# Kernel tuning notes

Measured on AMD Instinct MI355X. Metric: run time of the kernel, lower is better.

The kernel has to match this reference:

```python
import jax, jax.numpy as jnp
import numpy as np

FEAT = 1024
B = 1024
S = 64


def setup_inputs() -> dict:
    key = jax.random.key(0)
    ks = jax.random.split(key, 6)
    scale_ih = 1.0 / np.sqrt(2 * FEAT)
    scale_hh = 1.0 / np.sqrt(FEAT)
    return {
        "query": jax.random.normal(ks[0], (B, FEAT), jnp.float32) * 0.1,
        "support_context": jax.random.normal(ks[1], (S, FEAT), jnp.float32) * 0.1,
        "W_ih": jax.random.normal(ks[2], (4 * FEAT, 2 * FEAT), jnp.float32) * scale_ih,
        "W_hh": jax.random.normal(ks[3], (4 * FEAT, FEAT), jnp.float32) * scale_hh,
        "b_ih": jax.random.normal(ks[4], (4 * FEAT,), jnp.float32) * scale_hh,
        "b_hh": jax.random.normal(ks[5], (4 * FEAT,), jnp.float32) * scale_hh,
    }


def reference(query, support_context, W_ih, W_hh, b_ih, b_hh):
    # query: [B, F]; support_context: [S, F]; steps == S
    hidden = query
    cell = jnp.zeros_like(query)
    support_t = support_context.T  # [F, S]

    def step(carry, _):
        h, c = carry
        attn = jax.nn.softmax(h @ support_t, axis=1)          # [B, S]
        readout = attn @ support_context                      # [B, F]
        x = jnp.concatenate([query, readout], axis=1)         # [B, 2F]
        gates = x @ W_ih.T + b_ih + h @ W_hh.T + b_hh          # [B, 4F]
        i, f, g, o = jnp.split(gates, 4, axis=1)               # torch LSTMCell gate order
        c_new = jax.nn.sigmoid(f) * c + jax.nn.sigmoid(i) * jnp.tanh(g)
        h_new = jax.nn.sigmoid(o) * jnp.tanh(c_new) + query   # skip connection per original
        return (h_new, c_new), None

    (hidden, cell), _ = jax.lax.scan(step, (hidden, cell), None,
                                     length=support_context.shape[0])
    return hidden
```

## Files before the change

### kernel.cpp

```cpp
#include <hip/hip_runtime.h>
#include <hip/hip_bf16.h>


typedef __attribute__((ext_vector_type(8))) __bf16 bf16x8;
typedef __attribute__((ext_vector_type(4))) float f32x4;
typedef __attribute__((ext_vector_type(8))) unsigned short ushort8;

__device__ __forceinline__ ushort f2bf(float f) {
  union { float f; unsigned int u; } v; v.f = f;
  unsigned int u = v.u;
  u += 0x7FFFu + ((u >> 16) & 1u);
  return (ushort)(u >> 16);
}
__device__ __forceinline__ float bf2f(ushort u) {
  union { float f; unsigned int u; } v; v.u = ((unsigned int)u) << 16; return v.f;
}
__device__ __forceinline__ float sigm_(float x) { return 1.f / (1.f + __expf(-x)); }
__device__ __forceinline__ float tanh_(float x) {
  x = fminf(15.f, fmaxf(-15.f, x));
  float e = __expf(2.f * x);
  return (e - 1.f) / (e + 1.f);
}
__device__ __forceinline__ void async16(ushort* lds, const ushort* g) {
  __builtin_amdgcn_global_load_lds(
      (const __attribute__((address_space(1))) void*)g,
      (__attribute__((address_space(3))) void*)lds, 16, 0, 0);
}
__device__ __forceinline__ int permrow(int n) {
  int g = n >> 10, j = n & 1023;
  return ((j >> 4) << 6) | (g << 4) | (j & 15);
}

__global__ __launch_bounds__(256) void prep_kernel(
    const float* __restrict__ query, const float* __restrict__ support,
    const float* __restrict__ W_ih, const float* __restrict__ W_hh,
    const float* __restrict__ b_ih, const float* __restrict__ b_hh,
    ushort* __restrict__ Wq_bf, ushort* __restrict__ Wcomb,
    float* __restrict__ bias_p, ushort* __restrict__ X0,
    float* __restrict__ c, float* __restrict__ sT)
{
  int g = blockIdx.x * 256 + threadIdx.x;
  int n = g >> 10, k = g & 1023;
  int np = permrow(n);
  Wq_bf[(size_t)np * 1024 + k] = f2bf(W_ih[(size_t)n * 2048 + k]);
  Wcomb[(size_t)np * 1088 + k] = f2bf(W_hh[(size_t)n * 1024 + k]);
  if (g < 1024 * 1024) {
    X0[(size_t)(g >> 10) * 1088 + (g & 1023)] = f2bf(query[g]);
    c[g] = 0.f;
  }
  if (g < 4096) bias_p[permrow(g)] = b_ih[g] + b_hh[g];
  if (g < 65536) { int kk = g >> 6, s = g & 63; sT[g] = support[(size_t)s * 1024 + kk]; }
}

__global__ __launch_bounds__(256) void sw_kernel(
    const float* __restrict__ sT, const float* __restrict__ W_ih,
    ushort* __restrict__ Wcomb)
{
  int g = blockIdx.x * 256 + threadIdx.x;
  int n = g >> 6, s = g & 63;
  const float* wp = W_ih + (size_t)n * 2048 + 1024;
  const float* sp = sT + s;
  float a0 = 0.f, a1 = 0.f, a2 = 0.f, a3 = 0.f;
#pragma unroll 4
  for (int k = 0; k < 1024; k += 4) {
    a0 += wp[k]     * sp[(size_t)(k)     * 64];
    a1 += wp[k + 1] * sp[(size_t)(k + 1) * 64];
    a2 += wp[k + 2] * sp[(size_t)(k + 2) * 64];
    a3 += wp[k + 3] * sp[(size_t)(k + 3) * 64];
  }
  Wcomb[(size_t)permrow(n) * 1088 + 1024 + s] = f2bf((a0 + a1) + (a2 + a3));
}

__global__ __launch_bounds__(256) void attn_kernel(
    const ushort* __restrict__ Xh, const float* __restrict__ sT,
    ushort* __restrict__ Xa)
{
  __shared__ float hs[2][1024];
  __shared__ float part[4][2][64];
  int t = threadIdx.x;
  int b0 = blockIdx.x * 2;
  {
    int r = t >> 7, c8 = (t & 127) << 3;
    ushort8 v = *(const ushort8*)&Xh[(size_t)(b0 + r) * 1088 + c8];
#pragma unroll
    for (int i = 0; i < 8; i++) hs[r][c8 + i] = bf2f(v[i]);
  }
  __syncthreads();
  int s = t & 63, q = t >> 6;
  const float* st = sT + (size_t)q * 256 * 64 + s;
  const float* h0 = &hs[0][q * 256];
  const float* h1 = &hs[1][q * 256];
  float a0 = 0.f, a1 = 0.f;
#pragma unroll 8
  for (int k = 0; k < 256; k++) {
    float sv = st[(size_t)k * 64];
    a0 += h0[k] * sv; a1 += h1[k] * sv;
  }
  part[q][0][s] = a0; part[q][1][s] = a1;
  __syncthreads();
  if (t < 64) {
#pragma unroll
    for (int r = 0; r < 2; r++) {
      float v = part[0][r][t] + part[1][r][t] + part[2][r][t] + part[3][r][t];
      float m = v;
      for (int off = 32; off; off >>= 1) m = fmaxf(m, __shfl_xor(m, off));
      float e = __expf(v - m);
      float sm = e;
      for (int off = 32; off; off >>= 1) sm += __shfl_xor(sm, off);
      Xa[(size_t)(b0 + r) * 1088 + 1024 + t] = f2bf(e / sm);
    }
  }
}

__global__ __launch_bounds__(256) void gemm_step(
    const ushort* __restrict__ A, const ushort* __restrict__ Bw,
    int lda, int ldb, int K,
    const float* __restrict__ base, const float* __restrict__ bias,
    float* __restrict__ Cout,
    float* __restrict__ cbuf, const float* __restrict__ query,
    ushort* __restrict__ Xout, float* __restrict__ outp)
{
  __shared__ ushort As[3][64 * 32];
  __shared__ ushort Bs[3][128 * 32];
  const int t = threadIdx.x;
  const int bid = blockIdx.x;
  const int xcd = bid & 7, idx = bid >> 3;
  const int bx = idx & 15, byy = idx >> 4;
  const int by = xcd * 4 + byy;
  const int m0 = bx * 64, n0 = by * 128;
  const int w = t >> 6, l = t & 63;
  const int wm = (w >> 1) * 32, wn = (w & 1) * 64;
  const int srow = t >> 2, scol = (t & 3) * 8;
  const ushort* ga  = A  + (size_t)(m0 + srow) * lda + scol;
  const ushort* gb0 = Bw + (size_t)(n0 + srow) * ldb + scol;
  const ushort* gb1 = Bw + (size_t)(n0 + 64 + srow) * ldb + scol;
  const int fr = l & 15, fk = (l >> 4) * 8, fq = l >> 4;
  f32x4 acc[2][4] = {};
  const int nt = K >> 5;
  {
    async16(&As[0][t * 8], ga);
    async16(&Bs[0][t * 8], gb0);
    async16(&Bs[0][2048 + t * 8], gb1);
    async16(&As[1][t * 8], ga + 32);
    async16(&Bs[1][t * 8], gb0 + 32);
    async16(&Bs[1][2048 + t * 8], gb1 + 32);
  }
  for (int it = 0; it < nt; it++) {
    if (it + 1 < nt) { asm volatile("s_waitcnt vmcnt(3)" ::: "memory"); }
    else             { asm volatile("s_waitcnt vmcnt(0)" ::: "memory"); }
    __builtin_amdgcn_s_barrier();
    __builtin_amdgcn_sched_barrier(0);
    const int b = it % 3;
    const ushort* pa = &As[b][(wm + fr) * 32 + fk];
    const ushort* pb = &Bs[b][(wn + fr) * 32 + fk];
    bf16x8 af[2], bfv[4];
#pragma unroll
    for (int mi = 0; mi < 2; mi++) af[mi] = *(const bf16x8*)(pa + mi * 512);
#pragma unroll
    for (int ni = 0; ni < 4; ni++) bfv[ni] = *(const bf16x8*)(pb + ni * 512);
    if (it + 2 < nt) {
      const int pbuf = (it + 2) % 3;
      const int k0 = (it + 2) << 5;
      async16(&As[pbuf][t * 8], ga + k0);
      async16(&Bs[pbuf][t * 8], gb0 + k0);
      async16(&Bs[pbuf][2048 + t * 8], gb1 + k0);
    }
#pragma unroll
    for (int mi = 0; mi < 2; mi++)
#pragma unroll
      for (int ni = 0; ni < 4; ni++)
        acc[mi][ni] = __builtin_amdgcn_mfma_f32_16x16x32_bf16(af[mi], bfv[ni], acc[mi][ni], 0, 0, 0);
  }
  if (!base) {
#pragma unroll
    for (int mi = 0; mi < 2; mi++)
#pragma unroll
      for (int ni = 0; ni < 4; ni++) {
        int col = n0 + wn + ni * 16 + fr;
        int row0 = m0 + wm + mi * 16 + fq * 4;
        float bv = bias[col];
#pragma unroll
        for (int jj = 0; jj < 4; jj++)
          Cout[(size_t)(row0 + jj) * 4096 + col] = acc[mi][ni][jj] + bv;
      }
    return;
  }
  const int jbase = (((n0 + wn) >> 6) << 4);
  const int jcol = jbase + fr;
#pragma unroll
  for (int mi = 0; mi < 2; mi++) {
#pragma unroll
    for (int jj = 0; jj < 4; jj++) {
      int row = m0 + wm + mi * 16 + fq * 4 + jj;
      const float* bp = base + (size_t)row * 4096 + (n0 + wn);
      float gi = acc[mi][0][jj] + bp[fr];
      float gf = acc[mi][1][jj] + bp[16 + fr];
      float gg = acc[mi][2][jj] + bp[32 + fr];
      float go = acc[mi][3][jj] + bp[48 + fr];
      size_t cidx = (size_t)row * 1024 + jcol;
      float cv = cbuf[cidx];
      float cn = sigm_(gf) * cv + sigm_(gi) * tanh_(gg);
      float hn = sigm_(go) * tanh_(cn) + query[cidx];
      cbuf[cidx] = cn;
      Xout[(size_t)row * 1088 + jcol] = f2bf(hn);
      if (outp) outp[cidx] = hn;
    }
  }
}

extern "C" void kernel_launch(void* const* d_in, const int* in_sizes, int n_in,
                              void* d_out, int out_size, void* d_ws, size_t ws_size,
                              hipStream_t stream) {
  const float* query   = (const float*)d_in[0];
  const float* support = (const float*)d_in[1];
  const float* W_ih    = (const float*)d_in[2];
  const float* W_hh    = (const float*)d_in[3];
  const float* b_ih    = (const float*)d_in[4];
  const float* b_hh    = (const float*)d_in[5];
  float* out = (float*)d_out;

  char* ws = (char*)d_ws;
  size_t off = 0;
  auto alloc = [&](size_t bytes) {
    void* p = ws + off;
    off += (bytes + 255) & ~(size_t)255;
    return p;
  };
  ushort* Wq_bf  = (ushort*)alloc((size_t)4096 * 1024 * 2);
  ushort* Wcomb  = (ushort*)alloc((size_t)4096 * 1088 * 2);
  float*  bias_p = (float*) alloc((size_t)4096 * 4);
  float*  base   = (float*) alloc((size_t)1024 * 4096 * 4);
  ushort* X0     = (ushort*)alloc((size_t)1024 * 1088 * 2);
  ushort* X1     = (ushort*)alloc((size_t)1024 * 1088 * 2);
  float*  c      = (float*) alloc((size_t)1024 * 1024 * 4);
  float*  sT     = (float*) alloc((size_t)1024 * 64 * 4);

  prep_kernel<<<16384, 256, 0, stream>>>(query, support, W_ih, W_hh, b_ih, b_hh,
                                         Wq_bf, Wcomb, bias_p, X0, c, sT);
  sw_kernel<<<1024, 256, 0, stream>>>(sT, W_ih, Wcomb);
  gemm_step<<<512, 256, 0, stream>>>(X0, Wq_bf, 1088, 1024, 1024,
                                     nullptr, bias_p, base,
                                     nullptr, nullptr, nullptr, nullptr);
  for (int step = 0; step < 64; step++) {
    ushort* Xc = (step & 1) ? X1 : X0;
    ushort* Xn = (step & 1) ? X0 : X1;
    attn_kernel<<<512, 256, 0, stream>>>(Xc, sT, Xc);
    gemm_step<<<512, 256, 0, stream>>>(Xc, Wcomb, 1088, 1088, 1088,
                                       base, nullptr, nullptr,
                                       c, query, Xn,
                                       (step == 63) ? out : nullptr);
  }
}
```

Before: 2.176 ms.

## Enlarge GEMM tiles, use MFMA for support-weight fold, batch four rows per attention block

The per-step gemm_step tile grows from 64x128 to 128x128 with four MFMA row fragments per wave, halving the grid to 256 blocks and raising operand reuse per LDS load. The scalar sw_kernel that folds W_ih's readout half with the support matrix is replaced by a bf16 MFMA kernel, which needs extra bf16 copies of that weight and the support. attn_kernel now handles four batch rows per block with float4 LDS reads and all four waves doing softmax. The larger tiles cut parallelism to 256 blocks, about one per CU, which may leave latency less hidden.

```diff
diff --git a/kernel.cpp b/kernel.cpp
--- a/kernel.cpp
+++ b/kernel.cpp
@@ -37,78 +37,133 @@
     const float* __restrict__ b_ih, const float* __restrict__ b_hh,
     ushort* __restrict__ Wq_bf, ushort* __restrict__ Wcomb,
     float* __restrict__ bias_p, ushort* __restrict__ X0,
-    float* __restrict__ c, float* __restrict__ sT)
+    float* __restrict__ c, float* __restrict__ sT,
+    ushort* __restrict__ Wr_bf, ushort* __restrict__ Sb)
 {
   int g = blockIdx.x * 256 + threadIdx.x;
   int n = g >> 10, k = g & 1023;
   int np = permrow(n);
   Wq_bf[(size_t)np * 1024 + k] = f2bf(W_ih[(size_t)n * 2048 + k]);
+  Wr_bf[(size_t)n * 1024 + k]  = f2bf(W_ih[(size_t)n * 2048 + 1024 + k]);
   Wcomb[(size_t)np * 1088 + k] = f2bf(W_hh[(size_t)n * 1024 + k]);
   if (g < 1024 * 1024) {
     X0[(size_t)(g >> 10) * 1088 + (g & 1023)] = f2bf(query[g]);
     c[g] = 0.f;
   }
   if (g < 4096) bias_p[permrow(g)] = b_ih[g] + b_hh[g];
-  if (g < 65536) { int kk = g >> 6, s = g & 63; sT[g] = support[(size_t)s * 1024 + kk]; }
-}
-
-__global__ __launch_bounds__(256) void sw_kernel(
-    const float* __restrict__ sT, const float* __restrict__ W_ih,
+  if (g < 65536) {
+    int kk = g >> 6, s = g & 63;
+    float v = support[(size_t)s * 1024 + kk];
+    sT[g] = v;
+    Sb[(size_t)s * 1024 + kk] = f2bf(v);
+  }
+}
+
+__global__ __launch_bounds__(256) void sw_mfma(
+    const ushort* __restrict__ Wr, const ushort* __restrict__ Sb,
     ushort* __restrict__ Wcomb)
 {
-  int g = blockIdx.x * 256 + threadIdx.x;
-  int n = g >> 6, s = g & 63;
-  const float* wp = W_ih + (size_t)n * 2048 + 1024;
-  const float* sp = sT + s;
-  float a0 = 0.f, a1 = 0.f, a2 = 0.f, a3 = 0.f;
-#pragma unroll 4
-  for (int k = 0; k < 1024; k += 4) {
-    a0 += wp[k]     * sp[(size_t)(k)     * 64];
-    a1 += wp[k + 1] * sp[(size_t)(k + 1) * 64];
-    a2 += wp[k + 2] * sp[(size_t)(k + 2) * 64];
-    a3 += wp[k + 3] * sp[(size_t)(k + 3) * 64];
-  }
-  Wcomb[(size_t)permrow(n) * 1088 + 1024 + s] = f2bf((a0 + a1) + (a2 + a3));
+  __shared__ ushort As[3][128 * 32];
+  __shared__ ushort Bs[3][64 * 32];
+  const int t = threadIdx.x;
+  const int bm0 = blockIdx.x * 128;
+  const int w = t >> 6, l = t & 63;
+  const int wm = w * 32;
+  const int srow = t >> 2, scol = (t & 3) * 8;
+  const ushort* ga0 = Wr + (size_t)(bm0 + srow) * 1024 + scol;
+  const ushort* ga1 = Wr + (size_t)(bm0 + 64 + srow) * 1024 + scol;
+  const ushort* gb0 = Sb + (size_t)srow * 1024 + scol;
+  const int fr = l & 15, fk = (l >> 4) * 8, fq = l >> 4;
+  f32x4 acc[2][4] = {};
+  const int nt = 32;
+  async16(&As[0][t * 8], ga0); async16(&As[0][2048 + t * 8], ga1);
+  async16(&Bs[0][t * 8], gb0);
+  async16(&As[1][t * 8], ga0 + 32); async16(&As[1][2048 + t * 8], ga1 + 32);
+  async16(&Bs[1][t * 8], gb0 + 32);
+  for (int it = 0; it < nt; it++) {
+    if (it + 1 < nt) { asm volatile("s_waitcnt vmcnt(3)" ::: "memory"); }
+    else             { asm volatile("s_waitcnt vmcnt(0)" ::: "memory"); }
+    __builtin_amdgcn_s_barrier();
+    __builtin_amdgcn_sched_barrier(0);
+    const int b = it % 3;
+    const ushort* pa = &As[b][(wm + fr) * 32 + fk];
+    const ushort* pb = &Bs[b][fr * 32 + fk];
+    bf16x8 af[2], bfv[4];
+#pragma unroll
+    for (int mi = 0; mi < 2; mi++) af[mi] = *(const bf16x8*)(pa + mi * 512);
+#pragma unroll
+    for (int ni = 0; ni < 4; ni++) bfv[ni] = *(const bf16x8*)(pb + ni * 512);
+    if (it + 2 < nt) {
+      const int pbuf = (it + 2) % 3;
+      const int k0 = (it + 2) << 5;
+      async16(&As[pbuf][t * 8], ga0 + k0); async16(&As[pbuf][2048 + t * 8], ga1 + k0);
+      async16(&Bs[pbuf][t * 8], gb0 + k0);
+    }
+#pragma unroll
+    for (int mi = 0; mi < 2; mi++)
+#pragma unroll
+      for (int ni = 0; ni < 4; ni++)
+        acc[mi][ni] = __builtin_amdgcn_mfma_f32_16x16x32_bf16(af[mi], bfv[ni], acc[mi][ni], 0, 0, 0);
+  }
+#pragma unroll
+  for (int mi = 0; mi < 2; mi++)
+#pragma unroll
+    for (int ni = 0; ni < 4; ni++) {
+      int s = ni * 16 + fr;
+      int row0 = bm0 + wm + mi * 16 + fq * 4;
+#pragma unroll
+      for (int jj = 0; jj < 4; jj++)
+        Wcomb[(size_t)permrow(row0 + jj) * 1088 + 1024 + s] = f2bf(acc[mi][ni][jj]);
+    }
 }
 
 __global__ __launch_bounds__(256) void attn_kernel(
     const ushort* __restrict__ Xh, const float* __restrict__ sT,
     ushort* __restrict__ Xa)
 {
-  __shared__ float hs[2][1024];
-  __shared__ float part[4][2][64];
+  __shared__ float hs[4][1024];
+  __shared__ float part[4][4][64];
   int t = threadIdx.x;
-  int b0 = blockIdx.x * 2;
-  {
-    int r = t >> 7, c8 = (t & 127) << 3;
+  int b0 = blockIdx.x * 4;
+#pragma unroll
+  for (int i = 0; i < 2; i++) {
+    int r = i * 2 + (t >> 7), c8 = (t & 127) << 3;
     ushort8 v = *(const ushort8*)&Xh[(size_t)(b0 + r) * 1088 + c8];
 #pragma unroll
-    for (int i = 0; i < 8; i++) hs[r][c8 + i] = bf2f(v[i]);
+    for (int jj = 0; jj < 8; jj++) hs[r][c8 + jj] = bf2f(v[jj]);
   }
   __syncthreads();
   int s = t & 63, q = t >> 6;
   const float* st = sT + (size_t)q * 256 * 64 + s;
-  const float* h0 = &hs[0][q * 256];
-  const float* h1 = &hs[1][q * 256];
-  float a0 = 0.f, a1 = 0.f;
-#pragma unroll 8
-  for (int k = 0; k < 256; k++) {
-    float sv = st[(size_t)k * 64];
-    a0 += h0[k] * sv; a1 += h1[k] * sv;
-  }
-  part[q][0][s] = a0; part[q][1][s] = a1;
+  const float* hp0 = &hs[0][q * 256];
+  const float* hp1 = &hs[1][q * 256];
+  const float* hp2 = &hs[2][q * 256];
+  const float* hp3 = &hs[3][q * 256];
+  float a0 = 0.f, a1 = 0.f, a2 = 0.f, a3 = 0.f;
+#pragma unroll 4
+  for (int kk = 0; kk < 256; kk += 4) {
+    float s0 = st[(size_t)kk * 64], s1 = st[(size_t)(kk + 1) * 64];
+    float s2 = st[(size_t)(kk + 2) * 64], s3 = st[(size_t)(kk + 3) * 64];
+    float4 h0 = *(const float4*)&hp0[kk];
+    float4 h1 = *(const float4*)&hp1[kk];
+    float4 h2 = *(const float4*)&hp2[kk];
+    float4 h3 = *(const float4*)&hp3[kk];
+    a0 += h0.x * s0 + h0.y * s1 + h0.z * s2 + h0.w * s3;
+    a1 += h1.x * s0 + h1.y * s1 + h1.z * s2 + h1.w * s3;
+    a2 += h2.x * s0 + h2.y * s1 + h2.z * s2 + h2.w * s3;
+    a3 += h3.x * s0 + h3.y * s1 + h3.z * s2 + h3.w * s3;
+  }
+  part[q][0][s] = a0; part[q][1][s] = a1; part[q][2][s] = a2; part[q][3][s] = a3;
   __syncthreads();
-  if (t < 64) {
-#pragma unroll
-    for (int r = 0; r < 2; r++) {
-      float v = part[0][r][t] + part[1][r][t] + part[2][r][t] + part[3][r][t];
-      float m = v;
-      for (int off = 32; off; off >>= 1) m = fmaxf(m, __shfl_xor(m, off));
-      float e = __expf(v - m);
-      float sm = e;
-      for (int off = 32; off; off >>= 1) sm += __shfl_xor(sm, off);
-      Xa[(size_t)(b0 + r) * 1088 + 1024 + t] = f2bf(e / sm);
-    }
+  {
+    int r = t >> 6, s2 = t & 63;
+    float v = part[0][r][s2] + part[1][r][s2] + part[2][r][s2] + part[3][r][s2];
+    float m = v;
+    for (int off = 32; off; off >>= 1) m = fmaxf(m, __shfl_xor(m, off));
+    float e = __expf(v - m);
+    float sm = e;
+    for (int off = 32; off; off >>= 1) sm += __shfl_xor(sm, off);
+    Xa[(size_t)(b0 + r) * 1088 + 1024 + s2] = f2bf(e / sm);
   }
 }
 
@@ -120,60 +175,55 @@
     float* __restrict__ cbuf, const float* __restrict__ query,
     ushort* __restrict__ Xout, float* __restrict__ outp)
 {
-  __shared__ ushort As[3][64 * 32];
+  __shared__ ushort As[3][128 * 32];
   __shared__ ushort Bs[3][128 * 32];
   const int t = threadIdx.x;
   const int bid = blockIdx.x;
-  const int xcd = bid & 7, idx = bid >> 3;
-  const int bx = idx & 15, byy = idx >> 4;
-  const int by = xcd * 4 + byy;
-  const int m0 = bx * 64, n0 = by * 128;
+  const int xcd = bid & 7, i = bid >> 3;
+  const int by = xcd * 4 + (i >> 3), bx = i & 7;
+  const int m0 = bx * 128, n0 = by * 128;
   const int w = t >> 6, l = t & 63;
-  const int wm = (w >> 1) * 32, wn = (w & 1) * 64;
+  const int wm = (w >> 1) * 64, wn = (w & 1) * 64;
   const int srow = t >> 2, scol = (t & 3) * 8;
-  const ushort* ga  = A  + (size_t)(m0 + srow) * lda + scol;
+  const ushort* ga0 = A + (size_t)(m0 + srow) * lda + scol;
+  const ushort* ga1 = A + (size_t)(m0 + 64 + srow) * lda + scol;
   const ushort* gb0 = Bw + (size_t)(n0 + srow) * ldb + scol;
   const ushort* gb1 = Bw + (size_t)(n0 + 64 + srow) * ldb + scol;
   const int fr = l & 15, fk = (l >> 4) * 8, fq = l >> 4;
-  f32x4 acc[2][4] = {};
+  f32x4 acc[4][4] = {};
   const int nt = K >> 5;
-  {
-    async16(&As[0][t * 8], ga);
-    async16(&Bs[0][t * 8], gb0);
-    async16(&Bs[0][2048 + t * 8], gb1);
-    async16(&As[1][t * 8], ga + 32);
-    async16(&Bs[1][t * 8], gb0 + 32);
-    async16(&Bs[1][2048 + t * 8], gb1 + 32);
-  }
+  async16(&As[0][t * 8], ga0); async16(&As[0][2048 + t * 8], ga1);
+  async16(&Bs[0][t * 8], gb0); async16(&Bs[0][2048 + t * 8], gb1);
+  async16(&As[1][t * 8], ga0 + 32); async16(&As[1][2048 + t * 8], ga1 + 32);
+  async16(&Bs[1][t * 8], gb0 + 32); async16(&Bs[1][2048 + t * 8], gb1 + 32);
   for (int it = 0; it < nt; it++) {
-    if (it + 1 < nt) { asm volatile("s_waitcnt vmcnt(3)" ::: "memory"); }
+    if (it + 1 < nt) { asm volatile("s_waitcnt vmcnt(4)" ::: "memory"); }
     else             { asm volatile("s_waitcnt vmcnt(0)" ::: "memory"); }
     __builtin_amdgcn_s_barrier();
     __builtin_amdgcn_sched_barrier(0);
     const int b = it % 3;
     const ushort* pa = &As[b][(wm + fr) * 32 + fk];
     const ushort* pb = &Bs[b][(wn + fr) * 32 + fk];
-    bf16x8 af[2], bfv[4];
-#pragma unroll
-    for (int mi = 0; mi < 2; mi++) af[mi] = *(const bf16x8*)(pa + mi * 512);
+    bf16x8 af[4], bfv[4];
+#pragma unroll
+    for (int mi = 0; mi < 4; mi++) af[mi] = *(const bf16x8*)(pa + mi * 512);
 #pragma unroll
     for (int ni = 0; ni < 4; ni++) bfv[ni] = *(const bf16x8*)(pb + ni * 512);
     if (it + 2 < nt) {
       const int pbuf = (it + 2) % 3;
       const int k0 = (it + 2) << 5;
-      async16(&As[pbuf][t * 8], ga + k0);
-      async16(&Bs[pbuf][t * 8], gb0 + k0);
-      async16(&Bs[pbuf][2048 + t * 8], gb1 + k0);
+      async16(&As[pbuf][t * 8], ga0 + k0); async16(&As[pbuf][2048 + t * 8], ga1 + k0);
+      async16(&Bs[pbuf][t * 8], gb0 + k0); async16(&Bs[pbuf][2048 + t * 8], gb1 + k0);
     }
 #pragma unroll
-    for (int mi = 0; mi < 2; mi++)
+    for (int mi = 0; mi < 4; mi++)
 #pragma unroll
       for (int ni = 0; ni < 4; ni++)
         acc[mi][ni] = __builtin_amdgcn_mfma_f32_16x16x32_bf16(af[mi], bfv[ni], acc[mi][ni], 0, 0, 0);
   }
   if (!base) {
 #pragma unroll
-    for (int mi = 0; mi < 2; mi++)
+    for (int mi = 0; mi < 4; mi++)
 #pragma unroll
       for (int ni = 0; ni < 4; ni++) {
         int col = n0 + wn + ni * 16 + fr;
@@ -188,7 +238,7 @@
   const int jbase = (((n0 + wn) >> 6) << 4);
   const int jcol = jbase + fr;
 #pragma unroll
-  for (int mi = 0; mi < 2; mi++) {
+  for (int mi = 0; mi < 4; mi++) {
 #pragma unroll
     for (int jj = 0; jj < 4; jj++) {
       int row = m0 + wm + mi * 16 + fq * 4 + jj;
@@ -228,6 +278,8 @@
   };
   ushort* Wq_bf  = (ushort*)alloc((size_t)4096 * 1024 * 2);
   ushort* Wcomb  = (ushort*)alloc((size_t)4096 * 1088 * 2);
+  ushort* Wr_bf  = (ushort*)alloc((size_t)4096 * 1024 * 2);
+  ushort* Sb     = (ushort*)alloc((size_t)64 * 1024 * 2);
   float*  bias_p = (float*) alloc((size_t)4096 * 4);
   float*  base   = (float*) alloc((size_t)1024 * 4096 * 4);
   ushort* X0     = (ushort*)alloc((size_t)1024 * 1088 * 2);
@@ -236,16 +288,17 @@
   float*  sT     = (float*) alloc((size_t)1024 * 64 * 4);
 
   prep_kernel<<<16384, 256, 0, stream>>>(query, support, W_ih, W_hh, b_ih, b_hh,
-                                         Wq_bf, Wcomb, bias_p, X0, c, sT);
-  sw_kernel<<<1024, 256, 0, stream>>>(sT, W_ih, Wcomb);
-  gemm_step<<<512, 256, 0, stream>>>(X0, Wq_bf, 1088, 1024, 1024,
+                                         Wq_bf, Wcomb, bias_p, X0, c, sT,
+                                         Wr_bf, Sb);
+  sw_mfma<<<32, 256, 0, stream>>>(Wr_bf, Sb, Wcomb);
+  gemm_step<<<256, 256, 0, stream>>>(X0, Wq_bf, 1088, 1024, 1024,
                                      nullptr, bias_p, base,
                                      nullptr, nullptr, nullptr, nullptr);
   for (int step = 0; step < 64; step++) {
     ushort* Xc = (step & 1) ? X1 : X0;
     ushort* Xn = (step & 1) ? X0 : X1;
-    attn_kernel<<<512, 256, 0, stream>>>(Xc, sT, Xc);
-    gemm_step<<<512, 256, 0, stream>>>(Xc, Wcomb, 1088, 1088, 1088,
+    attn_kernel<<<256, 256, 0, stream>>>(Xc, sT, Xc);
+    gemm_step<<<256, 256, 0, stream>>>(Xc, Wcomb, 1088, 1088, 1088,
                                        base, nullptr, nullptr,
                                        c, query, Xn,
                                        (step == 63) ? out : nullptr);
```

Measured after the change: 2.221 ms. 1.02x slower.
